# Kernel tuning notes

Hardware: AMD Instinct MI355X
Metric: run time of the kernel (lower is better)

The kernel has to match this reference:

```python
import jax, jax.numpy as jnp
import numpy as np


def setup_inputs() -> dict:
    key = jax.random.key(0)
    k1, k2 = jax.random.split(key)
    B, H, W = 64, 1024, 1024
    output = jax.random.normal(k1, (B, H, W), dtype=jnp.float32)
    target = jax.random.normal(k2, (B, H, W), dtype=jnp.float32)
    return {"output": output, "target": target, "patch_size": 64}


def reference(output, target, patch_size):
    # output, target: [B, H, W]; tile into non-overlapping p x p patches,
    # per-patch mean |o - t|, max over patches per image, mean over batch.
    B, H, W = output.shape
    p = patch_size
    nh, nw = H // p, W // p
    diff = jnp.abs(output - target)                      # [B, H, W]
    # [B, nh, p, nw, p] -> per-patch mean over the two p axes
    patch_l1 = diff.reshape(B, nh, p, nw, p).mean(axis=(2, 4))  # [B, nh, nw]
    max_patch_loss = patch_l1.max(axis=(1, 2))           # [B]
    # original initializes max at 0; L1 >= 0 so max with 0 is a no-op, kept for fidelity
    max_patch_loss = jnp.maximum(max_patch_loss, 0.0)
    return max_patch_loss.mean()
```

## Files before the change

### kernel.cpp

```cpp
#include <hip/hip_runtime.h>

#define BATCH   64
#define HEIGHT  1024
#define WIDTH   1024
#define PSZ     64
#define NPH     16
#define NPW     16

__global__ __launch_bounds__(256) void patch_rowstrip_kernel(
    const float* __restrict__ out_p, const float* __restrict__ tgt_p,
    float* __restrict__ blk_max)
{
    const int blk  = blockIdx.x;
    const int img  = blk >> 4;
    const int prow = blk & 15;

    const size_t base = (size_t)img * (HEIGHT * (size_t)WIDTH)
                      + (size_t)prow * PSZ * WIDTH
                      + (size_t)threadIdx.x * 4;

    const float4* __restrict__ po = reinterpret_cast<const float4*>(out_p + base);
    const float4* __restrict__ pt = reinterpret_cast<const float4*>(tgt_p + base);
    const int row_stride_f4 = WIDTH / 4;

    float s0 = 0.f, s1 = 0.f;
#pragma unroll 8
    for (int r = 0; r < PSZ; ++r) {
        const float4 a = po[(size_t)r * row_stride_f4];
        const float4 c = pt[(size_t)r * row_stride_f4];
        s0 += fabsf(a.x - c.x) + fabsf(a.y - c.y);
        s1 += fabsf(a.z - c.z) + fabsf(a.w - c.w);
    }
    float s = s0 + s1;

#pragma unroll
    for (int off = 8; off > 0; off >>= 1)
        s += __shfl_down(s, off, 16);

    __shared__ float lds[NPW];
    if ((threadIdx.x & 15) == 0) lds[threadIdx.x >> 4] = s;
    __syncthreads();
    if (threadIdx.x == 0) {
        float m = lds[0];
#pragma unroll
        for (int i = 1; i < NPW; ++i) m = fmaxf(m, lds[i]);
        blk_max[blk] = m * (1.0f / (PSZ * PSZ));
    }
}

__global__ __launch_bounds__(256) void final_reduce_kernel(
    const float* __restrict__ blk_max, float* __restrict__ result)
{
    const int t = threadIdx.x;
    const float4 v = reinterpret_cast<const float4*>(blk_max)[t];
    float m = fmaxf(fmaxf(v.x, v.y), fmaxf(v.z, v.w));
    m = fmaxf(m, __shfl_down(m, 2, 4));
    m = fmaxf(m, __shfl_down(m, 1, 4));
    float contrib = ((t & 3) == 0) ? m : 0.0f;
#pragma unroll
    for (int off = 32; off > 0; off >>= 1)
        contrib += __shfl_down(contrib, off, 64);

    __shared__ float lds[4];
    if ((t & 63) == 0) lds[t >> 6] = contrib;
    __syncthreads();
    if (t == 0)
        result[0] = (lds[0] + lds[1] + lds[2] + lds[3]) * (1.0f / BATCH);
}

extern "C" void kernel_launch(void* const* d_in, const int* in_sizes, int n_in,
                              void* d_out, int out_size, void* d_ws, size_t ws_size,
                              hipStream_t stream) {
    const float* out_p = (const float*)d_in[0];
    const float* tgt_p = (const float*)d_in[1];
    float* blk_max = (float*)d_ws;
    float* result  = (float*)d_out;

    patch_rowstrip_kernel<<<BATCH * NPH, 256, 0, stream>>>(out_p, tgt_p, blk_max);
    final_reduce_kernel<<<1, 256, 0, stream>>>(blk_max, result);
}
```

Before: 504.8 us.

## Split patch strips into half-row blocks with staggered row start order

Each patch-row strip is now split across two blocks of 32 rows, doubling the grid from 1024 to 2048 blocks, and the per-patch partial sums are written to workspace. The final kernel adds the two halves per patch, takes the max per image and averages over the batch. Each block also starts its row loop at a hashed offset, meant to spread concurrent accesses across memory channels. The cost is twice the partial writes and a larger final reduction, and the rotated order may hurt DRAM page locality.

```diff
diff --git a/kernel.cpp b/kernel.cpp
--- a/kernel.cpp
+++ b/kernel.cpp
@@ -1,31 +1,39 @@
 #include <hip/hip_runtime.h>
 
-#define BATCH   64
-#define HEIGHT  1024
-#define WIDTH   1024
-#define PSZ     64
-#define NPH     16
-#define NPW     16
+#define BATCH     64
+#define HEIGHT    1024
+#define WIDTH     1024
+#define PSZ       64
+#define NPH       16
+#define NPW       16
+#define HALF_ROWS 32
+#define NBLK      (BATCH * NPH * 2)
 
-__global__ __launch_bounds__(256) void patch_rowstrip_kernel(
+__global__ __launch_bounds__(256) void patch_halfstrip_kernel(
     const float* __restrict__ out_p, const float* __restrict__ tgt_p,
-    float* __restrict__ blk_max)
+    float* __restrict__ part)
 {
     const int blk  = blockIdx.x;
-    const int img  = blk >> 4;
-    const int prow = blk & 15;
+    const int img  = blk >> 5;
+    const int rem  = blk & 31;
+    const int prow = rem >> 1;
+    const int half = rem & 1;
 
     const size_t base = (size_t)img * (HEIGHT * (size_t)WIDTH)
                       + (size_t)prow * PSZ * WIDTH
+                      + (size_t)half * HALF_ROWS * WIDTH
                       + (size_t)threadIdx.x * 4;
 
     const float4* __restrict__ po = reinterpret_cast<const float4*>(out_p + base);
     const float4* __restrict__ pt = reinterpret_cast<const float4*>(tgt_p + base);
     const int row_stride_f4 = WIDTH / 4;
 
+    const int r0 = (int)(((unsigned)blk * 2654435761u) >> 27);
+
     float s0 = 0.f, s1 = 0.f;
 #pragma unroll 8
-    for (int r = 0; r < PSZ; ++r) {
+    for (int i = 0; i < HALF_ROWS; ++i) {
+        const int r = (i + r0) & (HALF_ROWS - 1);
         const float4 a = po[(size_t)r * row_stride_f4];
         const float4 c = pt[(size_t)r * row_stride_f4];
         s0 += fabsf(a.x - c.x) + fabsf(a.y - c.y);
@@ -37,35 +45,50 @@
     for (int off = 8; off > 0; off >>= 1)
         s += __shfl_down(s, off, 16);
 
-    __shared__ float lds[NPW];
-    if ((threadIdx.x & 15) == 0) lds[threadIdx.x >> 4] = s;
-    __syncthreads();
-    if (threadIdx.x == 0) {
-        float m = lds[0];
-#pragma unroll
-        for (int i = 1; i < NPW; ++i) m = fmaxf(m, lds[i]);
-        blk_max[blk] = m * (1.0f / (PSZ * PSZ));
+    if ((threadIdx.x & 15) == 0) {
+        const int pcol = threadIdx.x >> 4;
+        part[(size_t)img * (NPH * NPW * 2) + half * (NPH * NPW)
+             + prow * NPW + pcol] = s;
     }
 }
 
-__global__ __launch_bounds__(256) void final_reduce_kernel(
-    const float* __restrict__ blk_max, float* __restrict__ result)
+__global__ __launch_bounds__(1024) void final_reduce_kernel(
+    const float* __restrict__ part, float* __restrict__ result)
 {
-    const int t = threadIdx.x;
-    const float4 v = reinterpret_cast<const float4*>(blk_max)[t];
-    float m = fmaxf(fmaxf(v.x, v.y), fmaxf(v.z, v.w));
-    m = fmaxf(m, __shfl_down(m, 2, 4));
-    m = fmaxf(m, __shfl_down(m, 1, 4));
-    float contrib = ((t & 3) == 0) ? m : 0.0f;
+    const int t   = threadIdx.x;
+    const int img = t >> 4;
+    const int j   = t & 15;
+
+    const float4* __restrict__ p =
+        reinterpret_cast<const float4*>(part) + img * 128 + j * 4;
+
+    float m = 0.0f;
+#pragma unroll
+    for (int q = 0; q < 4; ++q) {
+        const float4 a = p[q];
+        const float4 b = p[64 + q];
+        m = fmaxf(m, fmaxf(fmaxf(a.x + b.x, a.y + b.y),
+                           fmaxf(a.z + b.z, a.w + b.w)));
+    }
+
+#pragma unroll
+    for (int off = 8; off > 0; off >>= 1)
+        m = fmaxf(m, __shfl_down(m, off, 16));
+
+    float contrib = (j == 0) ? m * (1.0f / (PSZ * PSZ)) : 0.0f;
 #pragma unroll
     for (int off = 32; off > 0; off >>= 1)
         contrib += __shfl_down(contrib, off, 64);
 
-    __shared__ float lds[4];
+    __shared__ float lds[16];
     if ((t & 63) == 0) lds[t >> 6] = contrib;
     __syncthreads();
-    if (t == 0)
-        result[0] = (lds[0] + lds[1] + lds[2] + lds[3]) * (1.0f / BATCH);
+    if (t == 0) {
+        float acc = 0.f;
+#pragma unroll
+        for (int i = 0; i < 16; ++i) acc += lds[i];
+        result[0] = acc * (1.0f / BATCH);
+    }
 }
 
 extern "C" void kernel_launch(void* const* d_in, const int* in_sizes, int n_in,
@@ -73,9 +96,9 @@
                               hipStream_t stream) {
     const float* out_p = (const float*)d_in[0];
     const float* tgt_p = (const float*)d_in[1];
-    float* blk_max = (float*)d_ws;
-    float* result  = (float*)d_out;
+    float* part   = (float*)d_ws;
+    float* result = (float*)d_out;
 
-    patch_rowstrip_kernel<<<BATCH * NPH, 256, 0, stream>>>(out_p, tgt_p, blk_max);
-    final_reduce_kernel<<<1, 256, 0, stream>>>(blk_max, result);
+    patch_halfstrip_kernel<<<NBLK, 256, 0, stream>>>(out_p, tgt_p, part);
+    final_reduce_kernel<<<1, 1024, 0, stream>>>(part, result);
 }
```

Result: no change. 507.6 us (+0.5%).

## Split patch reduction into per-row partial sums with grid-strided sweep

Applied to the files above, without the earlier changes.

Replaces the per-patch-row-strip kernel (1024 blocks, each summing 64 rows) with a 2048-block kernel where each block processes rows strided across the whole tensor, writing per-row, per-patch-column partial sums to workspace using nontemporal loads. A second kernel sums the 64 row partials per patch and takes the per-image max, and a third averages over the batch. This aims to raise block count and memory-level parallelism on the dominant streaming read, at the cost of an extra 4 MB workspace round trip and one more kernel launch.

```diff
diff --git a/kernel.cpp b/kernel.cpp
--- a/kernel.cpp
+++ b/kernel.cpp
@@ -6,66 +6,73 @@
 #define PSZ     64
 #define NPH     16
 #define NPW     16
+#define NROWS   (BATCH * HEIGHT)
+#define NBLK    2048
+#define K_STEPS (NROWS / NBLK)
 
-__global__ __launch_bounds__(256) void patch_rowstrip_kernel(
+using f32x4 = __attribute__((ext_vector_type(4))) float;
+
+__global__ __launch_bounds__(256) void rowsum_sweep_kernel(
     const float* __restrict__ out_p, const float* __restrict__ tgt_p,
-    float* __restrict__ blk_max)
+    float* __restrict__ rowsum)
 {
-    const int blk  = blockIdx.x;
-    const int img  = blk >> 4;
-    const int prow = blk & 15;
+    const int tid  = threadIdx.x;
+    const int pcol = tid >> 4;
+    const f32x4* __restrict__ po = reinterpret_cast<const f32x4*>(out_p);
+    const f32x4* __restrict__ pt = reinterpret_cast<const f32x4*>(tgt_p);
 
-    const size_t base = (size_t)img * (HEIGHT * (size_t)WIDTH)
-                      + (size_t)prow * PSZ * WIDTH
-                      + (size_t)threadIdx.x * 4;
-
-    const float4* __restrict__ po = reinterpret_cast<const float4*>(out_p + base);
-    const float4* __restrict__ pt = reinterpret_cast<const float4*>(tgt_p + base);
-    const int row_stride_f4 = WIDTH / 4;
-
-    float s0 = 0.f, s1 = 0.f;
-#pragma unroll 8
-    for (int r = 0; r < PSZ; ++r) {
-        const float4 a = po[(size_t)r * row_stride_f4];
-        const float4 c = pt[(size_t)r * row_stride_f4];
-        s0 += fabsf(a.x - c.x) + fabsf(a.y - c.y);
-        s1 += fabsf(a.z - c.z) + fabsf(a.w - c.w);
-    }
-    float s = s0 + s1;
-
+#pragma unroll 4
+    for (int k = 0; k < K_STEPS; ++k) {
+        const int row = (k << 11) + (int)blockIdx.x;
+        const size_t idx = (size_t)row * (WIDTH / 4) + tid;
+        const f32x4 a = __builtin_nontemporal_load(po + idx);
+        const f32x4 c = __builtin_nontemporal_load(pt + idx);
+        float s = fabsf(a[0] - c[0]) + fabsf(a[1] - c[1])
+                + fabsf(a[2] - c[2]) + fabsf(a[3] - c[3]);
 #pragma unroll
-    for (int off = 8; off > 0; off >>= 1)
-        s += __shfl_down(s, off, 16);
-
-    __shared__ float lds[NPW];
-    if ((threadIdx.x & 15) == 0) lds[threadIdx.x >> 4] = s;
-    __syncthreads();
-    if (threadIdx.x == 0) {
-        float m = lds[0];
-#pragma unroll
-        for (int i = 1; i < NPW; ++i) m = fmaxf(m, lds[i]);
-        blk_max[blk] = m * (1.0f / (PSZ * PSZ));
+        for (int off = 8; off > 0; off >>= 1)
+            s += __shfl_down(s, off, 16);
+        if ((tid & 15) == 0)
+            rowsum[(size_t)row * NPW + pcol] = s;
     }
 }
 
-__global__ __launch_bounds__(256) void final_reduce_kernel(
-    const float* __restrict__ blk_max, float* __restrict__ result)
+__global__ __launch_bounds__(256) void img_max_kernel(
+    const float* __restrict__ rowsum, float* __restrict__ img_max)
 {
-    const int t = threadIdx.x;
-    const float4 v = reinterpret_cast<const float4*>(blk_max)[t];
-    float m = fmaxf(fmaxf(v.x, v.y), fmaxf(v.z, v.w));
-    m = fmaxf(m, __shfl_down(m, 2, 4));
-    m = fmaxf(m, __shfl_down(m, 1, 4));
-    float contrib = ((t & 3) == 0) ? m : 0.0f;
+    const int img = blockIdx.x;
+    const int t   = threadIdx.x;
+    const float* __restrict__ base =
+        rowsum + ((size_t)img * NPH + (t >> 4)) * (PSZ * NPW) + (t & 15);
+
+    float s = 0.0f;
+#pragma unroll
+    for (int rip = 0; rip < PSZ; ++rip)
+        s += base[(size_t)rip * NPW];
+
+    float m = s;
 #pragma unroll
     for (int off = 32; off > 0; off >>= 1)
-        contrib += __shfl_down(contrib, off, 64);
+        m = fmaxf(m, __shfl_down(m, off, 64));
 
     __shared__ float lds[4];
-    if ((t & 63) == 0) lds[t >> 6] = contrib;
+    if ((t & 63) == 0) lds[t >> 6] = m;
     __syncthreads();
-    if (t == 0)
-        result[0] = (lds[0] + lds[1] + lds[2] + lds[3]) * (1.0f / BATCH);
+    if (t == 0) {
+        float v = fmaxf(fmaxf(lds[0], lds[1]), fmaxf(lds[2], lds[3]));
+        img_max[img] = v * (1.0f / (PSZ * PSZ));
+    }
+}
+
+__global__ __launch_bounds__(64) void final_mean_kernel(
+    const float* __restrict__ img_max, float* __restrict__ result)
+{
+    float v = img_max[threadIdx.x];
+#pragma unroll
+    for (int off = 32; off > 0; off >>= 1)
+        v += __shfl_down(v, off, 64);
+    if (threadIdx.x == 0)
+        result[0] = v * (1.0f / BATCH);
 }
 
 extern "C" void kernel_launch(void* const* d_in, const int* in_sizes, int n_in,
@@ -73,9 +80,11 @@
                               hipStream_t stream) {
     const float* out_p = (const float*)d_in[0];
     const float* tgt_p = (const float*)d_in[1];
-    float* blk_max = (float*)d_ws;
+    float* rowsum  = (float*)d_ws;
+    float* img_max = (float*)d_ws + (size_t)NROWS * NPW;
     float* result  = (float*)d_out;
 
-    patch_rowstrip_kernel<<<BATCH * NPH, 256, 0, stream>>>(out_p, tgt_p, blk_max);
-    final_reduce_kernel<<<1, 256, 0, stream>>>(blk_max, result);
+    rowsum_sweep_kernel<<<NBLK, 256, 0, stream>>>(out_p, tgt_p, rowsum);
+    img_max_kernel<<<BATCH, 256, 0, stream>>>(rowsum, img_max);
+    final_mean_kernel<<<1, 64, 0, stream>>>(img_max, result);
 }
```

Measured after the change: 494.7 us. 1.02x faster.
